# Performance work log

Hardware: AMD Instinct MI355X
Metric: run time of the kernel (lower is better)

## Reference

```python
import jax, jax.numpy as jnp
import numpy as np

B, T, C = 1, 2048, 1024
H = 16
HD = C // H
BLOCK = 2048
NEG = float('-inf')

def setup_inputs() -> dict:
    key = jax.random.key(0)
    ks = jax.random.split(key, 6)
    x = jax.random.normal(ks[0], (B, T, C), dtype=jnp.float32)
    cumulative_scores = jax.random.normal(ks[1], (B, T), dtype=jnp.float32) * 0.1
    padding_mask = jnp.ones((B, T), dtype=jnp.float32)
    token_index = jax.random.randint(ks[2], (B, T), 0, BLOCK).astype(jnp.int64)
    w_attn = jax.random.normal(ks[3], (C, 3 * C), dtype=jnp.float32) * (1.0 / np.sqrt(C))
    b_attn = jnp.zeros((3 * C,), dtype=jnp.float32)
    w_proj = jax.random.normal(ks[4], (C, C), dtype=jnp.float32) * (1.0 / np.sqrt(C))
    b_proj = jnp.zeros((C,), dtype=jnp.float32)
    return dict(x=x, cumulative_scores=cumulative_scores, padding_mask=padding_mask,
                token_index=token_index, w_attn=w_attn, b_attn=b_attn,
                w_proj=w_proj, b_proj=b_proj)

def _rotate_half(z):
    z1, z2 = z[..., : z.shape[-1] // 2], z[..., z.shape[-1] // 2 :]
    return jnp.concatenate((-z2, z1), axis=-1)

def reference(x, cumulative_scores, padding_mask, token_index, w_attn, b_attn, w_proj, b_proj):
    # fused QKV projection
    qkv = x @ w_attn + b_attn                      # (B,T,3C)
    q, k, v = jnp.split(qkv, 3, axis=2)
    q = q.reshape(B, T, H, HD).transpose(0, 2, 1, 3)  # (B,H,T,HD)
    k = k.reshape(B, T, H, HD).transpose(0, 2, 1, 3)
    v = v.reshape(B, T, H, HD).transpose(0, 2, 1, 3)

    # dynamic per-token RoPE positions: global token counts (original scatter
    # broadcasts indices over batch, so counts are global across all batches)
    cnt = jnp.zeros((BLOCK,), jnp.float32).at[token_index.reshape(-1)].add(1.0)
    per_tok = (1.0 / (cnt + 1e-10))[token_index]       # (B,T)
    partial = jnp.cumsum(per_tok, axis=-1)             # (B,T) fractional positions

    inv_freq = 1.0 / (10000.0 ** (jnp.arange(0, HD, 2, dtype=jnp.float32) / HD))
    freqs = partial[..., None] * inv_freq              # (B,T,HD/2)
    emb = jnp.concatenate((freqs, freqs), axis=-1)     # (B,T,HD)
    cos = jnp.cos(emb)[:, None]                        # (B,1,T,HD)
    sin = jnp.sin(emb)[:, None]
    q = q * cos + _rotate_half(q) * sin
    k = k * cos + _rotate_half(k) * sin

    # 'fork' plan: overwrite last channel
    q = q.at[..., -1].set(1.0)
    k = k.at[..., -1].set(jnp.broadcast_to(cumulative_scores[:, None, :], (B, H, T)))

    # additive causal + padding mask (B,T,T)
    causal = jnp.where(jnp.tril(jnp.ones((T, T), jnp.bool_)), 0.0, NEG)
    pm = jnp.take_along_axis(padding_mask, token_index, axis=1)     # (B,T)
    outer = pm[:, :, None] * pm[:, None, :]
    pad_add = jnp.where(outer.astype(jnp.bool_), 0.0, NEG)
    mask = causal[None, :, :] + pad_add                              # (B,T,T)

    # scale v by exp(cumulative_scores)
    v = v * jnp.exp(cumulative_scores)[:, None, :, None]

    scores = jnp.einsum('bhqd,bhkd->bhqk', q, k) / np.sqrt(HD) + mask[:, None]
    probs = jax.nn.softmax(scores, axis=-1)
    y = jnp.einsum('bhqk,bhkd->bhqd', probs, v)        # (B,H,T,HD)
    y = y.transpose(0, 2, 1, 3).reshape(B, T, C)
    return y @ w_proj + b_proj
```

## Files before the change

### kernel.cpp

```cpp
#include <hip/hip_runtime.h>
#include <math.h>

#define T 2048
#define C 1024
#define H 16
#define HD 64
#define N3 (3*C)
#define NBLOCK 2048

typedef __attribute__((ext_vector_type(8))) short bf16x8;
typedef __attribute__((ext_vector_type(4))) float f32x4;

#define MFMA16(a, b, c) __builtin_amdgcn_mfma_f32_16x16x32_bf16((a), (b), (c), 0, 0, 0)

__device__ inline short f2bf(float f) {
    unsigned u; __builtin_memcpy(&u, &f, 4);
    unsigned r = (u + 0x7fffu + ((u >> 16) & 1u)) >> 16;
    return (short)r;
}
__device__ inline float bf2f(short s) {
    unsigned u = ((unsigned)(unsigned short)s) << 16;
    float f; __builtin_memcpy(&f, &u, 4);
    return f;
}

__device__ inline void gload_lds16(const void* g, void* l) {
    __builtin_amdgcn_global_load_lds((const __attribute__((address_space(1))) unsigned int*)g,
                                     (__attribute__((address_space(3))) unsigned int*)l,
                                     16, 0, 0);
}

__global__ __launch_bounds__(256) void pre_kernel(const float* __restrict__ x,
                                                  const float* __restrict__ w_attn,
                                                  const float* __restrict__ w_proj,
                                                  const int* __restrict__ tok,
                                                  const float* __restrict__ padmask,
                                                  short* __restrict__ xb,
                                                  short* __restrict__ wabT,
                                                  short* __restrict__ wpbT,
                                                  float* __restrict__ partial,
                                                  float* __restrict__ pm_tok) {
    int bid = blockIdx.x;
    int tid = threadIdx.x;
    if (bid == 3072) {
        __shared__ float cntS[NBLOCK];
        __shared__ float sums[256];
        #pragma unroll
        for (int j = 0; j < 8; ++j) cntS[tid * 8 + j] = 0.0f;
        __syncthreads();
        int tk[8];
        #pragma unroll
        for (int j = 0; j < 8; ++j) {
            tk[j] = tok[tid * 8 + j];
            atomicAdd(&cntS[tk[j]], 1.0f);
        }
        __syncthreads();
        float vals[8];
        float s = 0.0f;
        #pragma unroll
        for (int j = 0; j < 8; ++j) {
            s += 1.0f / (cntS[tk[j]] + 1e-10f);
            vals[j] = s;
            pm_tok[tid * 8 + j] = padmask[tk[j]];
        }
        sums[tid] = s;
        __syncthreads();
        for (int off = 1; off < 256; off <<= 1) {
            float v = (tid >= off) ? sums[tid - off] : 0.0f;
            __syncthreads();
            sums[tid] += v;
            __syncthreads();
        }
        float offset = (tid > 0) ? sums[tid - 1] : 0.0f;
        #pragma unroll
        for (int j = 0; j < 8; ++j) partial[tid * 8 + j] = offset + vals[j];
        return;
    }
    if (bid < 2048) {
        int i = bid * 1024 + tid * 4;
        float4 v = *(const float4*)(x + i);
        short4 o;
        o.x = f2bf(v.x); o.y = f2bf(v.y); o.z = f2bf(v.z); o.w = f2bf(v.w);
        *(short4*)(xb + i) = o;
        return;
    }
    __shared__ float S[64][65];
    const float* in; short* out; int Kd, Nd, bx, by;
    if (bid < 2816) {
        int b = bid - 2048;
        bx = b % 48; by = b / 48;
        in = w_attn; out = wabT; Kd = C; Nd = N3;
    } else {
        int b = bid - 2816;
        bx = b % 16; by = b / 16;
        in = w_proj; out = wpbT; Kd = C; Nd = C;
    }
    int n0 = bx * 64, k0 = by * 64;
    #pragma unroll
    for (int i = 0; i < 16; ++i) {
        int lin = tid + i * 256;
        int r = lin >> 6, c = lin & 63;
        S[r][c] = in[(size_t)(k0 + r) * Nd + n0 + c];
    }
    __syncthreads();
    #pragma unroll
    for (int i = 0; i < 16; ++i) {
        int lin = tid + i * 256;
        int rn = lin >> 6, ck = lin & 63;
        out[(size_t)(n0 + rn) * Kd + k0 + ck] = f2bf(S[ck][rn]);
    }
}

template <int OUT_BF16, int EPI>
__global__ __launch_bounds__(256) void gemm_bt64(const short* __restrict__ A,
                                                 const short* __restrict__ Bt,
                                                 const float* __restrict__ bias,
                                                 void* __restrict__ Cout,
                                                 int M, int N, int K,
                                                 const float* __restrict__ partial,
                                                 const float* __restrict__ cumsc,
                                                 const float* __restrict__ pm_tok,
                                                 short* __restrict__ vbT) {
    __shared__ alignas(16) short As[2][2][64 * 32];
    __shared__ alignas(16) short Bs[2][2][128 * 32];
    int tid = threadIdx.x;
    int nwg = gridDim.x * gridDim.y;
    int bidl = blockIdx.y * gridDim.x + blockIdx.x;
    int swz = (bidl & 7) * (nwg >> 3) + (bidl >> 3);
    int m0 = (swz / gridDim.x) * 64, n0 = (swz % gridDim.x) * 128;
    int w = tid >> 6, l = tid & 63;
    int wm = (w >> 1) * 32, wn = (w & 1) * 64;
    int lq = l & 15, g = l >> 4;
    int prow = l >> 2, pcol = (l & 3) * 8;
    f32x4 acc[2][4] = {};

    auto stage = [&](int ph, int k0) {
        #pragma unroll
        for (int hf = 0; hf < 2; ++hf) {
            int kk = k0 + hf * 32;
            int rowA = w * 16 + prow;
            gload_lds16(A + (size_t)(m0 + rowA) * K + kk + pcol, As[ph][hf] + w * 512);
            #pragma unroll
            for (int i = 0; i < 2; ++i) {
                int c = w * 2 + i;
                int row = c * 16 + prow;
                gload_lds16(Bt + (size_t)(n0 + row) * K + kk + pcol, Bs[ph][hf] + c * 512);
            }
        }
    };

    int NK = K / 64;
    stage(0, 0);
    __syncthreads();
    for (int t = 0; t < NK; ++t) {
        int ph = t & 1;
        if (t + 1 < NK) stage(ph ^ 1, (t + 1) * 64);
        #pragma unroll
        for (int hf = 0; hf < 2; ++hf) {
            bf16x8 af[2], bfr[4];
            #pragma unroll
            for (int f = 0; f < 2; ++f)
                af[f] = *(const bf16x8*)(As[ph][hf] + (wm + f * 16 + lq) * 32 + g * 8);
            #pragma unroll
            for (int j = 0; j < 4; ++j)
                bfr[j] = *(const bf16x8*)(Bs[ph][hf] + (wn + j * 16 + lq) * 32 + g * 8);
            #pragma unroll
            for (int fi = 0; fi < 2; ++fi)
                #pragma unroll
                for (int fj = 0; fj < 4; ++fj)
                    acc[fi][fj] = MFMA16(af[fi], bfr[fj], acc[fi][fj]);
        }
        __syncthreads();
    }

    if (EPI == 0) {
        #pragma unroll
        for (int fi = 0; fi < 2; ++fi)
            #pragma unroll
            for (int fj = 0; fj < 4; ++fj)
                #pragma unroll
                for (int r = 0; r < 4; ++r) {
                    int m = m0 + wm + fi * 16 + g * 4 + r;
                    int n = n0 + wn + fj * 16 + lq;
                    float v = acc[fi][fj][r] + bias[n];
                    if (OUT_BF16) ((short*)Cout)[(size_t)m * N + n] = f2bf(v);
                    else          ((float*)Cout)[(size_t)m * N + n] = v;
                }
    } else {
        short* Cb = (short*)Cout;
        int cb = n0 + wn;
        int section = cb >> 10;
        float b0 = bias[cb + lq],      b1 = bias[cb + 16 + lq];
        float b2 = bias[cb + 32 + lq], b3 = bias[cb + 48 + lq];
        if (section < 2) {
            bool isQ = (section == 0);
            float inv0 = exp2f(-(float)lq * (13.287712379549449f / 32.0f));
            float inv1 = exp2f(-(float)(lq + 16) * (13.287712379549449f / 32.0f));
            #pragma unroll
            for (int fi = 0; fi < 2; ++fi)
                #pragma unroll
                for (int r = 0; r < 4; ++r) {
                    int trow = m0 + wm + fi * 16 + g * 4 + r;
                    float pt = partial[trow];
                    float sn0, cs0, sn1, cs1;
                    __sincosf(pt * inv0, &sn0, &cs0);
                    __sincosf(pt * inv1, &sn1, &cs1);
                    float a0 = acc[fi][0][r] + b0;
                    float a1 = acc[fi][1][r] + b1;
                    float a2 = acc[fi][2][r] + b2;
                    float a3 = acc[fi][3][r] + b3;
                    float lo0 = a0 * cs0 - a2 * sn0;
                    float hi0 = a2 * cs0 + a0 * sn0;
                    float lo1 = a1 * cs1 - a3 * sn1;
                    float hi1 = a3 * cs1 + a1 * sn1;
                    if (lq == 15) {
                        float pm = pm_tok[trow];
                        hi1 = isQ ? ((pm != 0.0f) ? 1.0f : 0.0f)
                                  : ((pm != 0.0f) ? cumsc[trow] : -1e20f);
                    }
                    size_t base = (size_t)trow * N3 + cb;
                    Cb[base + lq]      = f2bf(lo0);
                    Cb[base + 16 + lq] = f2bf(lo1);
                    Cb[base + 32 + lq] = f2bf(hi0);
                    Cb[base + 48 + lq] = f2bf(hi1);
                }
        } else {
            int h = (cb - 2 * C) >> 6;
            #pragma unroll
            for (int fi = 0; fi < 2; ++fi) {
                int tb = m0 + wm + fi * 16 + g * 4;
                float ef[4];
                #pragma unroll
                for (int r = 0; r < 4; ++r) ef[r] = __expf(cumsc[tb + r]);
                #pragma unroll
                for (int fj = 0; fj < 4; ++fj) {
                    int d = fj * 16 + lq;
                    float bv = (fj == 0) ? b0 : (fj == 1) ? b1 : (fj == 2) ? b2 : b3;
                    short4 o;
                    o.x = f2bf((acc[fi][fj][0] + bv) * ef[0]);
                    o.y = f2bf((acc[fi][fj][1] + bv) * ef[1]);
                    o.z = f2bf((acc[fi][fj][2] + bv) * ef[2]);
                    o.w = f2bf((acc[fi][fj][3] + bv) * ef[3]);
                    *(short4*)(vbT + (size_t)(h * 64 + d) * T + tb) = o;
                }
            }
        }
    }
}

__global__ __launch_bounds__(256) void attn_flash(const short* __restrict__ qkvb,
                                                  const short* __restrict__ vbT,
                                                  short* __restrict__ yb,
                                                  float* __restrict__ Opart,
                                                  float* __restrict__ Lpart) {
    __shared__ alignas(16) short Kt[2][64 * 64];
    __shared__ alignas(16) short Vt[2][64 * 64];
    __shared__ alignas(16) short Ps[4][16][72];

    int b = blockIdx.x;
    int h, qt, t0, t1, mode;
    if (b < 256)      { h = b & 15; qt = 16 + (b >> 4); t0 = 0;  t1 = 16; mode = 1; }
    else if (b < 512) { int c = b - 256; h = c & 15; qt = 31 - (c >> 4); t0 = 17; t1 = qt; mode = 2; }
    else              { int c = b - 512; h = c & 15; qt = c >> 4; t0 = 0; t1 = qt; mode = 0; }
    int nt = t1 - t0 + 1;

    int tid = threadIdx.x;
    int w = tid >> 6, l = tid & 63;
    int lq = l & 15, g = l >> 4;
    int qrl = w * 16 + lq;
    int qrow = qt * 64 + qrl;

    const short* qbase = qkvb + (size_t)qrow * N3 + h * 64;
    bf16x8 qf0 = *(const bf16x8*)(qbase + g * 8);
    bf16x8 qf1 = *(const bf16x8*)(qbase + 32 + g * 8);

    f32x4 accO[4] = {};
    float lsum = 0.0f;

    int srow = tid >> 3, scol = (tid & 7) * 8;
    const short* kgb = qkvb + C + h * 64 + scol;
    const short* vgb = vbT + (size_t)(h * 64) * T + scol;
    int wb0 = srow * 128 + ((scol * 2) ^ ((srow & 7) << 4));
    int wb1 = (srow + 32) * 128 + ((scol * 2) ^ ((srow & 7) << 4));

    uint4 kr0, kr1, vr0, vr1;
    auto stageRegs = [&](int tile) {
        int kb = tile * 64;
        kr0 = *(const uint4*)(kgb + (size_t)(kb + srow) * N3);
        kr1 = *(const uint4*)(kgb + (size_t)(kb + srow + 32) * N3);
        vr0 = *(const uint4*)(vgb + (size_t)srow * T + kb);
        vr1 = *(const uint4*)(vgb + (size_t)(srow + 32) * T + kb);
    };
    auto writeLds = [&](int buf) {
        *(uint4*)((char*)Kt[buf] + wb0) = kr0;
        *(uint4*)((char*)Kt[buf] + wb1) = kr1;
        *(uint4*)((char*)Vt[buf] + wb0) = vr0;
        *(uint4*)((char*)Vt[buf] + wb1) = vr1;
    };

    auto do_tile = [&](int buf, bool masked) {
        const char* Kc = (const char*)Kt[buf];
        const char* Vc = (const char*)Vt[buf];
        f32x4 s[4] = {};
        __builtin_amdgcn_s_setprio(1);
        #pragma unroll
        for (int f = 0; f < 4; ++f) {
            int row = f * 16 + lq;
            const char* kr_ = Kc + row * 128;
            int sw = (row & 7) << 4;
            bf16x8 a0 = *(const bf16x8*)(kr_ + ((g * 16) ^ sw));
            bf16x8 a1 = *(const bf16x8*)(kr_ + ((64 + g * 16) ^ sw));
            s[f] = MFMA16(a0, qf0, s[f]);
            s[f] = MFMA16(a1, qf1, s[f]);
        }
        __builtin_amdgcn_s_setprio(0);
        float p[16];
        #pragma unroll
        for (int f = 0; f < 4; ++f)
            #pragma unroll
            for (int r = 0; r < 4; ++r) {
                float sv = s[f][r] * 0.125f;
                if (masked) {
                    int kl = f * 16 + g * 4 + r;
                    sv = (kl > qrl) ? -INFINITY : sv;
                }
                float pv = __expf(sv);
                p[f * 4 + r] = pv;
                lsum += pv;
            }
        #pragma unroll
        for (int f = 0; f < 4; ++f) {
            unsigned u0, u1;
            asm("v_cvt_pk_bf16_f32 %0, %1, %2" : "=v"(u0) : "v"(p[f * 4 + 0]), "v"(p[f * 4 + 1]));
            asm("v_cvt_pk_bf16_f32 %0, %1, %2" : "=v"(u1) : "v"(p[f * 4 + 2]), "v"(p[f * 4 + 3]));
            uint2 uu; uu.x = u0; uu.y = u1;
            *(uint2*)&Ps[w][lq][f * 16 + g * 4] = uu;
        }
        __builtin_amdgcn_s_setprio(1);
        #pragma unroll
        for (int kh = 0; kh < 2; ++kh) {
            bf16x8 pa = *(const bf16x8*)&Ps[w][lq][kh * 32 + g * 8];
            #pragma unroll
            for (int f = 0; f < 4; ++f) {
                int vrow = f * 16 + lq;
                const char* vr_ = Vc + vrow * 128;
                bf16x8 vb = *(const bf16x8*)(vr_ + (((kh * 32 + g * 8) * 2) ^ ((vrow & 7) << 4)));
                accO[f] = MFMA16(pa, vb, accO[f]);
            }
        }
        __builtin_amdgcn_s_setprio(0);
    };

    if (nt > 0) { stageRegs(t0); writeLds(0); }
    __syncthreads();

    for (int j = 0; j < nt; ++j) {
        int t = t0 + j;
        bool pf = (j + 1 < nt);
        if (pf) stageRegs(t + 1);
        do_tile(j & 1, t == qt);
        if (pf) writeLds((j & 1) ^ 1);
        __syncthreads();
    }

    lsum += __shfl_xor(lsum, 16);
    lsum += __shfl_xor(lsum, 32);

    if (mode == 0) {
        float linv_own = 1.0f / lsum;
        float li[4];
        #pragma unroll
        for (int r = 0; r < 4; ++r) li[r] = __shfl(linv_own, g * 4 + r);
        #pragma unroll
        for (int f = 0; f < 4; ++f)
            #pragma unroll
            for (int r = 0; r < 4; ++r) {
                int trow = qt * 64 + w * 16 + g * 4 + r;
                yb[(size_t)trow * C + h * 64 + f * 16 + lq] = f2bf(accO[f][r] * li[r]);
            }
    } else {
        int kh = mode - 1;
        int slab = h * 16 + (qt - 16);
        float* Ob = Opart + ((size_t)kh * 256 + slab) * 4096;
        #pragma unroll
        for (int f = 0; f < 4; ++f)
            #pragma unroll
            for (int r = 0; r < 4; ++r)
                Ob[(w * 16 + g * 4 + r) * 64 + f * 16 + lq] = accO[f][r];
        if (g == 0) Lpart[((size_t)kh * 256 + slab) * 64 + w * 16 + lq] = lsum;
    }
}

__global__ __launch_bounds__(256) void attn_combine(const float* __restrict__ Opart,
                                                    const float* __restrict__ Lpart,
                                                    short* __restrict__ yb) {
    __shared__ float linvS[64];
    int s = blockIdx.x;
    int h = s >> 4, qt = 16 + (s & 15);
    int tid = threadIdx.x;
    if (tid < 64)
        linvS[tid] = 1.0f / (Lpart[(size_t)s * 64 + tid] + Lpart[(size_t)(256 + s) * 64 + tid]);
    __syncthreads();
    const float* O0 = Opart + (size_t)s * 4096;
    const float* O1 = Opart + (size_t)(256 + s) * 4096;
    #pragma unroll
    for (int e = 0; e < 4; ++e) {
        int base = tid * 4 + e * 1024;
        float4 a = *(const float4*)(O0 + base);
        float4 c = *(const float4*)(O1 + base);
        int q = base >> 6, d = base & 63;
        float li = linvS[q];
        short4 o;
        o.x = f2bf((a.x + c.x) * li);
        o.y = f2bf((a.y + c.y) * li);
        o.z = f2bf((a.z + c.z) * li);
        o.w = f2bf((a.w + c.w) * li);
        *(short4*)(yb + (size_t)(qt * 64 + q) * C + h * 64 + d) = o;
    }
}

extern "C" void kernel_launch(void* const* d_in, const int* in_sizes, int n_in,
                              void* d_out, int out_size, void* d_ws, size_t ws_size,
                              hipStream_t stream) {
    const float* x       = (const float*)d_in[0];
    const float* cumsc   = (const float*)d_in[1];
    const float* padmask = (const float*)d_in[2];
    const int*   tok     = (const int*)d_in[3];
    const float* w_attn  = (const float*)d_in[4];
    const float* b_attn  = (const float*)d_in[5];
    const float* w_proj  = (const float*)d_in[6];
    const float* b_proj  = (const float*)d_in[7];
    float* out = (float*)d_out;

    float* part   = (float*)d_ws;
    float* pm_tok = part + 2048;
    float* Opart  = pm_tok + 2048;
    float* Lpart  = Opart + (size_t)2 * 256 * 4096;
    short* xb     = (short*)(Lpart + 2 * 256 * 64);
    short* wabT   = xb + (size_t)T * C;
    short* wpbT   = wabT + (size_t)N3 * C;
    short* qkvb   = wpbT + (size_t)C * C;
    short* vbT    = qkvb + (size_t)T * N3;
    short* yb     = vbT + (size_t)C * T;

    pre_kernel<<<3073, 256, 0, stream>>>(x, w_attn, w_proj, tok, padmask,
                                         xb, wabT, wpbT, part, pm_tok);
    gemm_bt64<1, 1><<<dim3(N3 / 128, T / 64), 256, 0, stream>>>(
        xb, wabT, b_attn, qkvb, T, N3, C, part, cumsc, pm_tok, vbT);
    attn_flash<<<768, 256, 0, stream>>>(qkvb, vbT, yb, Opart, Lpart);
    attn_combine<<<256, 256, 0, stream>>>(Opart, Lpart, yb);
    gemm_bt64<0, 0><<<dim3(C / 128, T / 64), 256, 0, stream>>>(
        yb, wpbT, b_proj, out, T, C, C, nullptr, nullptr, nullptr, nullptr);
}
```

Baseline: 80.45 us.

## Use 2 waves with 32 query rows each and direct global-to-LDS K/V loads

The flash-attention kernel drops from 4 waves of 16 query rows to 2 waves of 32 query rows each. Each K and V fragment read from LDS is now reused for two MFMAs. K/V staging switches from register-staged loads plus LDS writes to a gload_lds16 direct global-to-LDS path, using the XOR swizzle applied on the global column index. This cuts LDS read traffic and VGPR staging per tile, but doubles accumulator registers per wave and halves threads per block, which may lower latency hiding.

```diff
diff --git a/kernel.cpp b/kernel.cpp
--- a/kernel.cpp
+++ b/kernel.cpp
@@ -248,14 +248,14 @@
     }
 }
 
-__global__ __launch_bounds__(256) void attn_flash(const short* __restrict__ qkvb,
+__global__ __launch_bounds__(128) void attn_flash(const short* __restrict__ qkvb,
                                                   const short* __restrict__ vbT,
                                                   short* __restrict__ yb,
                                                   float* __restrict__ Opart,
                                                   float* __restrict__ Lpart) {
     __shared__ alignas(16) short Kt[2][64 * 64];
     __shared__ alignas(16) short Vt[2][64 * 64];
-    __shared__ alignas(16) short Ps[4][16][72];
+    __shared__ alignas(16) short Ps[2][32][72];
 
     int b = blockIdx.x;
     int h, qt, t0, t1, mode;
@@ -267,41 +267,38 @@
     int tid = threadIdx.x;
     int w = tid >> 6, l = tid & 63;
     int lq = l & 15, g = l >> 4;
-    int qrl = w * 16 + lq;
-    int qrow = qt * 64 + qrl;
-
-    const short* qbase = qkvb + (size_t)qrow * N3 + h * 64;
-    bf16x8 qf0 = *(const bf16x8*)(qbase + g * 8);
-    bf16x8 qf1 = *(const bf16x8*)(qbase + 32 + g * 8);
-
-    f32x4 accO[4] = {};
-    float lsum = 0.0f;
-
-    int srow = tid >> 3, scol = (tid & 7) * 8;
-    const short* kgb = qkvb + C + h * 64 + scol;
-    const short* vgb = vbT + (size_t)(h * 64) * T + scol;
-    int wb0 = srow * 128 + ((scol * 2) ^ ((srow & 7) << 4));
-    int wb1 = (srow + 32) * 128 + ((scol * 2) ^ ((srow & 7) << 4));
-
-    uint4 kr0, kr1, vr0, vr1;
-    auto stageRegs = [&](int tile) {
+
+    bf16x8 q0f[2], q1f[2];
+    #pragma unroll
+    for (int qf = 0; qf < 2; ++qf) {
+        const short* qbase = qkvb + (size_t)(qt * 64 + w * 32 + qf * 16 + lq) * N3 + h * 64;
+        q0f[qf] = *(const bf16x8*)(qbase + g * 8);
+        q1f[qf] = *(const bf16x8*)(qbase + 32 + g * 8);
+    }
+
+    f32x4 accO[4][2] = {};
+    float lsum0 = 0.0f, lsum1 = 0.0f;
+
+    int lrow = l >> 3;
+    int colS = ((l & 7) ^ lrow) * 8;
+    const short* kgb = qkvb + C + h * 64 + colS;
+    const short* vgb = vbT + (size_t)(h * 64) * T;
+
+    auto stage = [&](int buf, int tile) {
         int kb = tile * 64;
-        kr0 = *(const uint4*)(kgb + (size_t)(kb + srow) * N3);
-        kr1 = *(const uint4*)(kgb + (size_t)(kb + srow + 32) * N3);
-        vr0 = *(const uint4*)(vgb + (size_t)srow * T + kb);
-        vr1 = *(const uint4*)(vgb + (size_t)(srow + 32) * T + kb);
-    };
-    auto writeLds = [&](int buf) {
-        *(uint4*)((char*)Kt[buf] + wb0) = kr0;
-        *(uint4*)((char*)Kt[buf] + wb1) = kr1;
-        *(uint4*)((char*)Vt[buf] + wb0) = vr0;
-        *(uint4*)((char*)Vt[buf] + wb1) = vr1;
+        #pragma unroll
+        for (int j = 0; j < 4; ++j) {
+            int c = w * 4 + j;
+            int row = c * 8 + lrow;
+            gload_lds16(kgb + (size_t)(kb + row) * N3, Kt[buf] + c * 512);
+            gload_lds16(vgb + (size_t)row * T + kb + colS, Vt[buf] + c * 512);
+        }
     };
 
     auto do_tile = [&](int buf, bool masked) {
         const char* Kc = (const char*)Kt[buf];
         const char* Vc = (const char*)Vt[buf];
-        f32x4 s[4] = {};
+        f32x4 s[4][2] = {};
         __builtin_amdgcn_s_setprio(1);
         #pragma unroll
         for (int f = 0; f < 4; ++f) {
@@ -310,73 +307,87 @@
             int sw = (row & 7) << 4;
             bf16x8 a0 = *(const bf16x8*)(kr_ + ((g * 16) ^ sw));
             bf16x8 a1 = *(const bf16x8*)(kr_ + ((64 + g * 16) ^ sw));
-            s[f] = MFMA16(a0, qf0, s[f]);
-            s[f] = MFMA16(a1, qf1, s[f]);
+            s[f][0] = MFMA16(a0, q0f[0], s[f][0]);
+            s[f][0] = MFMA16(a1, q1f[0], s[f][0]);
+            s[f][1] = MFMA16(a0, q0f[1], s[f][1]);
+            s[f][1] = MFMA16(a1, q1f[1], s[f][1]);
         }
         __builtin_amdgcn_s_setprio(0);
-        float p[16];
-        #pragma unroll
-        for (int f = 0; f < 4; ++f)
-            #pragma unroll
-            for (int r = 0; r < 4; ++r) {
-                float sv = s[f][r] * 0.125f;
-                if (masked) {
-                    int kl = f * 16 + g * 4 + r;
-                    sv = (kl > qrl) ? -INFINITY : sv;
+        #pragma unroll
+        for (int qf = 0; qf < 2; ++qf) {
+            int qrl = w * 32 + qf * 16 + lq;
+            float p[16];
+            float ls = 0.0f;
+            #pragma unroll
+            for (int f = 0; f < 4; ++f)
+                #pragma unroll
+                for (int r = 0; r < 4; ++r) {
+                    float sv = s[f][qf][r] * 0.125f;
+                    if (masked) {
+                        int kl = f * 16 + g * 4 + r;
+                        sv = (kl > qrl) ? -INFINITY : sv;
+                    }
+                    float pv = __expf(sv);
+                    p[f * 4 + r] = pv;
+                    ls += pv;
                 }
-                float pv = __expf(sv);
-                p[f * 4 + r] = pv;
-                lsum += pv;
-            }
-        #pragma unroll
-        for (int f = 0; f < 4; ++f) {
-            unsigned u0, u1;
-            asm("v_cvt_pk_bf16_f32 %0, %1, %2" : "=v"(u0) : "v"(p[f * 4 + 0]), "v"(p[f * 4 + 1]));
-            asm("v_cvt_pk_bf16_f32 %0, %1, %2" : "=v"(u1) : "v"(p[f * 4 + 2]), "v"(p[f * 4 + 3]));
-            uint2 uu; uu.x = u0; uu.y = u1;
-            *(uint2*)&Ps[w][lq][f * 16 + g * 4] = uu;
+            if (qf == 0) lsum0 += ls; else lsum1 += ls;
+            #pragma unroll
+            for (int f = 0; f < 4; ++f) {
+                unsigned u0, u1;
+                asm("v_cvt_pk_bf16_f32 %0, %1, %2" : "=v"(u0) : "v"(p[f * 4 + 0]), "v"(p[f * 4 + 1]));
+                asm("v_cvt_pk_bf16_f32 %0, %1, %2" : "=v"(u1) : "v"(p[f * 4 + 2]), "v"(p[f * 4 + 3]));
+                uint2 uu; uu.x = u0; uu.y = u1;
+                *(uint2*)&Ps[w][qf * 16 + lq][f * 16 + g * 4] = uu;
+            }
         }
         __builtin_amdgcn_s_setprio(1);
         #pragma unroll
         for (int kh = 0; kh < 2; ++kh) {
-            bf16x8 pa = *(const bf16x8*)&Ps[w][lq][kh * 32 + g * 8];
+            bf16x8 pa0 = *(const bf16x8*)&Ps[w][lq][kh * 32 + g * 8];
+            bf16x8 pa1 = *(const bf16x8*)&Ps[w][16 + lq][kh * 32 + g * 8];
             #pragma unroll
             for (int f = 0; f < 4; ++f) {
                 int vrow = f * 16 + lq;
                 const char* vr_ = Vc + vrow * 128;
                 bf16x8 vb = *(const bf16x8*)(vr_ + (((kh * 32 + g * 8) * 2) ^ ((vrow & 7) << 4)));
-                accO[f] = MFMA16(pa, vb, accO[f]);
+                accO[f][0] = MFMA16(pa0, vb, accO[f][0]);
+                accO[f][1] = MFMA16(pa1, vb, accO[f][1]);
             }
         }
         __builtin_amdgcn_s_setprio(0);
     };
 
-    if (nt > 0) { stageRegs(t0); writeLds(0); }
+    if (nt > 0) stage(0, t0);
     __syncthreads();
 
     for (int j = 0; j < nt; ++j) {
-        int t = t0 + j;
-        bool pf = (j + 1 < nt);
-        if (pf) stageRegs(t + 1);
-        do_tile(j & 1, t == qt);
-        if (pf) writeLds((j & 1) ^ 1);
+        if (j + 1 < nt) stage((j & 1) ^ 1, t0 + j + 1);
+        do_tile(j & 1, (t0 + j) == qt);
         __syncthreads();
     }
 
-    lsum += __shfl_xor(lsum, 16);
-    lsum += __shfl_xor(lsum, 32);
+    lsum0 += __shfl_xor(lsum0, 16);
+    lsum0 += __shfl_xor(lsum0, 32);
+    lsum1 += __shfl_xor(lsum1, 16);
+    lsum1 += __shfl_xor(lsum1, 32);
 
     if (mode == 0) {
-        float linv_own = 1.0f / lsum;
-        float li[4];
-        #pragma unroll
-        for (int r = 0; r < 4; ++r) li[r] = __shfl(linv_own, g * 4 + r);
+        float inv0 = 1.0f / lsum0, inv1 = 1.0f / lsum1;
+        float li0[4], li1[4];
+        #pragma unroll
+        for (int r = 0; r < 4; ++r) {
+            li0[r] = __shfl(inv0, g * 4 + r);
+            li1[r] = __shfl(inv1, g * 4 + r);
+        }
         #pragma unroll
         for (int f = 0; f < 4; ++f)
             #pragma unroll
             for (int r = 0; r < 4; ++r) {
-                int trow = qt * 64 + w * 16 + g * 4 + r;
-                yb[(size_t)trow * C + h * 64 + f * 16 + lq] = f2bf(accO[f][r] * li[r]);
+                int tr0 = qt * 64 + w * 32 + g * 4 + r;
+                int tr1 = tr0 + 16;
+                yb[(size_t)tr0 * C + h * 64 + f * 16 + lq] = f2bf(accO[f][0][r] * li0[r]);
+                yb[(size_t)tr1 * C + h * 64 + f * 16 + lq] = f2bf(accO[f][1][r] * li1[r]);
             }
     } else {
         int kh = mode - 1;
@@ -385,9 +396,14 @@
         #pragma unroll
         for (int f = 0; f < 4; ++f)
             #pragma unroll
-            for (int r = 0; r < 4; ++r)
-                Ob[(w * 16 + g * 4 + r) * 64 + f * 16 + lq] = accO[f][r];
-        if (g == 0) Lpart[((size_t)kh * 256 + slab) * 64 + w * 16 + lq] = lsum;
+            for (int r = 0; r < 4; ++r) {
+                Ob[(w * 32 + g * 4 + r) * 64 + f * 16 + lq]      = accO[f][0][r];
+                Ob[(w * 32 + 16 + g * 4 + r) * 64 + f * 16 + lq] = accO[f][1][r];
+            }
+        if (g == 0) {
+            Lpart[((size_t)kh * 256 + slab) * 64 + w * 32 + lq]      = lsum0;
+            Lpart[((size_t)kh * 256 + slab) * 64 + w * 32 + 16 + lq] = lsum1;
+        }
     }
 }
 
@@ -447,7 +463,7 @@
                                          xb, wabT, wpbT, part, pm_tok);
     gemm_bt64<1, 1><<<dim3(N3 / 128, T / 64), 256, 0, stream>>>(
         xb, wabT, b_attn, qkvb, T, N3, C, part, cumsc, pm_tok, vbT);
-    attn_flash<<<768, 256, 0, stream>>>(qkvb, vbT, yb, Opart, Lpart);
+    attn_flash<<<768, 128, 0, stream>>>(qkvb, vbT, yb, Opart, Lpart);
     attn_combine<<<256, 256, 0, stream>>>(Opart, Lpart, yb);
     gemm_bt64<0, 0><<<dim3(C / 128, T / 64), 256, 0, stream>>>(
         yb, wpbT, b_proj, out, T, C, C, nullptr, nullptr, nullptr, nullptr);
```

Result: slower. 85.74 us (+6.6%).
